# Kernel optimization log

Hardware: AMD Instinct MI355X
Metric: run time of the kernel (lower is better)

Reference implementation:

```python
import jax, jax.numpy as jnp
import numpy as np

IN_CH, OUT_CH, K, DIL = 64, 128, 3, 8

def setup_inputs() -> dict:
    key = jax.random.key(0)
    k1, k2, k3 = jax.random.split(key, 3)
    x = jax.random.normal(k1, (16, IN_CH, 128, 128), dtype=jnp.float32)
    # xavier_normal-like init for W
    fan_in, fan_out = IN_CH * K * K, OUT_CH * K * K
    std = (2.0 / (fan_in + fan_out)) ** 0.5
    W = jax.random.normal(k2, (OUT_CH, IN_CH, K, K), dtype=jnp.float32) * std
    b = jax.random.normal(k3, (OUT_CH,), dtype=jnp.float32)
    return {"x": x, "W": W, "b": b}

def reference(x, W, b):
    pad = DIL * (K // 2)  # circular halo so output spatial size == input
    xp = jnp.pad(x, ((0, 0), (0, 0), (pad, pad), (pad, pad)), mode="wrap")
    y = jax.lax.conv_general_dilated(
        xp, W,
        window_strides=(1, 1),
        padding="VALID",
        rhs_dilation=(DIL, DIL),
        dimension_numbers=("NCHW", "OIHW", "NCHW"),
    )
    return y + b[None, :, None, None]
```

## Files before the change

### kernel.cpp

```cpp
#include <hip/hip_runtime.h>

#define IN_CH 64
#define OUT_CH 128
#define HW 128
#define KTAPS 9
#define ROWB 16384

typedef __bf16 bf16x8 __attribute__((ext_vector_type(8)));
typedef float f32x16 __attribute__((ext_vector_type(16)));
typedef float f32x4 __attribute__((ext_vector_type(4)));

__device__ __forceinline__ unsigned f2bf(float f) {
    unsigned u = __builtin_bit_cast(unsigned, f);
    return (u + 0x7FFFu + ((u >> 16) & 1u)) >> 16;
}

__device__ __forceinline__ unsigned cvt_pk_bf16(float lo, float hi) {
    unsigned r;
    asm("v_cvt_pk_bf16_f32 %0, %1, %2" : "=v"(r) : "v"(lo), "v"(hi));
    return r;
}

__device__ __forceinline__ int swz(int r) { return ((r ^ (r >> 3)) & 7) << 4; }

__global__ void wprep_kernel(const float* __restrict__ W, unsigned short* __restrict__ Wl) {
    int i = blockIdx.x * blockDim.x + threadIdx.x;
    if (i >= OUT_CH * IN_CH * KTAPS) return;
    int p  = i / 36864;
    int r  = i % 36864;
    int t  = r >> 12;
    int r2 = r & 4095;
    int m  = r2 >> 11;
    int ks = (r2 >> 9) & 3;
    int l  = (r2 >> 3) & 63;
    int e  = r2 & 7;
    int oc = p * 64 + m * 32 + (l & 31);
    int ic = ks * 16 + (l >> 5) * 8 + e;
    int kh = t / 3, kw = t % 3;
    Wl[i] = (unsigned short)f2bf(W[((oc * IN_CH + ic) * 3 + kh) * 3 + kw]);
}

#define ISSUE_A(B0, B1, B2, B3, T) do {                                              \
    const char* _pp = (const char*)Ab + (T) * 8192;                                  \
    asm volatile("global_load_dwordx4 %0, %1, off"             : "=v"(B0) : "v"(_pp)); \
    asm volatile("global_load_dwordx4 %0, %1, off offset:1024" : "=v"(B1) : "v"(_pp)); \
    asm volatile("global_load_dwordx4 %0, %1, off offset:2048" : "=v"(B2) : "v"(_pp)); \
    asm volatile("global_load_dwordx4 %0, %1, off offset:3072" : "=v"(B3) : "v"(_pp)); \
} while (0)

#define TAP_BODY(A0_, A1_, A2_, A3_, T, WAITSTR) do {                                \
    constexpr int _kh = (T) / 3, _kw = (T) % 3;                                      \
    int _xc0 = (wc * 64 + l31 + 8 * _kw - 8) & 127;                                  \
    int _xc1 = (_xc0 + 32) & 127;                                                    \
    int _b0 = _kh * ROWB + _xc0 * 128 + lhi * 16, _s0 = swz(_xc0);                   \
    int _b1 = _kh * ROWB + _xc1 * 128 + lhi * 16, _s1 = swz(_xc1);                   \
    asm volatile(WAITSTR);                                                           \
    __builtin_amdgcn_sched_barrier(0);                                               \
    const bf16x8 _A[4] = {A0_, A1_, A2_, A3_};                                       \
    _Pragma("unroll")                                                                \
    for (int ks = 0; ks < 4; ++ks) {                                                 \
        bf16x8 _vb0 = *reinterpret_cast<const bf16x8*>(xsB + ((_b0 + ks * 32) ^ _s0)); \
        bf16x8 _vb1 = *reinterpret_cast<const bf16x8*>(xsB + ((_b1 + ks * 32) ^ _s1)); \
        acc[0] = __builtin_amdgcn_mfma_f32_32x32x16_bf16(_A[ks], _vb0, acc[0], 0, 0, 0); \
        acc[1] = __builtin_amdgcn_mfma_f32_32x32x16_bf16(_A[ks], _vb1, acc[1], 0, 0, 0); \
    }                                                                                \
} while (0)

__global__ __launch_bounds__(512, 5) void conv_kernel_f(
    const float* __restrict__ x, const unsigned short* __restrict__ Wl,
    const float* __restrict__ bias, float* __restrict__ y)
{
    __shared__ __align__(16) unsigned char xsB[3 * ROWB];

    int bid = blockIdx.x;
    int sb  = (bid & 7) * 256 + (bid >> 3);
    int n = sb >> 7, h = sb & 127;
    int tid = threadIdx.x;
    int wid = tid >> 6, lane = tid & 63;

    int wr = wid >> 1, wc = wid & 1;
    int l31 = lane & 31, lhi = lane >> 5;
    int p = wr >> 1, m = wr & 1;

    const bf16x8* Ab = reinterpret_cast<const bf16x8*>(Wl)
                     + p * (9 * 512) + m * 256 + lane;

    bf16x8 aE0, aE1, aE2, aE3, aO0, aO1, aO2, aO3;
    ISSUE_A(aE0, aE1, aE2, aE3, 0);

    #pragma unroll
    for (int g = 0; g < 3; ++g) {
        int q   = g * 512 + tid;
        int w4  = q & 31;
        int ic4 = (q >> 5) & 15;
        int kh  = q >> 9;
        int srow = (h + kh * 8 + 120) & 127;
        const float* xp = x + (((n * IN_CH + ic4 * 4) * HW + srow) * HW + w4 * 4);
        f32x4 v[4];
        #pragma unroll
        for (int j = 0; j < 4; ++j)
            v[j] = *reinterpret_cast<const f32x4*>(xp + j * (HW * HW));
        #pragma unroll
        for (int j2 = 0; j2 < 4; ++j2) {
            int w = w4 * 4 + j2;
            uint2 pk;
            pk.x = cvt_pk_bf16(v[0][j2], v[1][j2]);
            pk.y = cvt_pk_bf16(v[2][j2], v[3][j2]);
            *reinterpret_cast<uint2*>(xsB + kh * ROWB + ((w * 128 + ic4 * 8) ^ swz(w))) = pk;
        }
    }
    __syncthreads();

    f32x16 acc[2];
    #pragma unroll
    for (int bq = 0; bq < 2; ++bq)
        #pragma unroll
        for (int r = 0; r < 16; ++r) acc[bq][r] = 0.0f;

    ISSUE_A(aO0, aO1, aO2, aO3, 1);
    TAP_BODY(aE0, aE1, aE2, aE3, 0, "s_waitcnt vmcnt(4)");
    ISSUE_A(aE0, aE1, aE2, aE3, 2);
    TAP_BODY(aO0, aO1, aO2, aO3, 1, "s_waitcnt vmcnt(4)");
    ISSUE_A(aO0, aO1, aO2, aO3, 3);
    TAP_BODY(aE0, aE1, aE2, aE3, 2, "s_waitcnt vmcnt(4)");
    ISSUE_A(aE0, aE1, aE2, aE3, 4);
    TAP_BODY(aO0, aO1, aO2, aO3, 3, "s_waitcnt vmcnt(4)");
    ISSUE_A(aO0, aO1, aO2, aO3, 5);
    TAP_BODY(aE0, aE1, aE2, aE3, 4, "s_waitcnt vmcnt(4)");
    ISSUE_A(aE0, aE1, aE2, aE3, 6);
    TAP_BODY(aO0, aO1, aO2, aO3, 5, "s_waitcnt vmcnt(4)");
    ISSUE_A(aO0, aO1, aO2, aO3, 7);
    TAP_BODY(aE0, aE1, aE2, aE3, 6, "s_waitcnt vmcnt(4)");
    ISSUE_A(aE0, aE1, aE2, aE3, 8);
    TAP_BODY(aO0, aO1, aO2, aO3, 7, "s_waitcnt vmcnt(4)");
    TAP_BODY(aE0, aE1, aE2, aE3, 8, "s_waitcnt vmcnt(0)");

    int outbase = (n * OUT_CH) * HW * HW + h * HW;
    #pragma unroll
    for (int bq = 0; bq < 2; ++bq) {
        int wcol = wc * 64 + bq * 32 + l31;
        #pragma unroll
        for (int reg = 0; reg < 16; ++reg) {
            int oc = wr * 32 + (reg & 3) + 8 * (reg >> 2) + 4 * lhi;
            y[outbase + oc * HW * HW + wcol] = acc[bq][reg] + bias[oc];
        }
    }
}

extern "C" void kernel_launch(void* const* d_in, const int* in_sizes, int n_in,
                              void* d_out, int out_size, void* d_ws, size_t ws_size,
                              hipStream_t stream) {
    const float* x = (const float*)d_in[0];
    const float* W = (const float*)d_in[1];
    const float* b = (const float*)d_in[2];
    float* y = (float*)d_out;

    unsigned short* Wl = (unsigned short*)d_ws;

    hipLaunchKernelGGL(wprep_kernel, dim3((OUT_CH * IN_CH * KTAPS + 255) / 256), dim3(256), 0, stream, W, Wl);
    hipLaunchKernelGGL(conv_kernel_f, dim3(16 * HW), dim3(512), 0, stream, x, Wl, b, y);
}
```

Measured before the change: 61.22 us.

## Split each output row into two half-row blocks with an 80-column halo tile

```diff
diff --git a/kernel.cpp b/kernel.cpp
--- a/kernel.cpp
+++ b/kernel.cpp
@@ -4,7 +4,8 @@
 #define OUT_CH 128
 #define HW 128
 #define KTAPS 9
-#define ROWB 16384
+#define LCOLS 80
+#define LROWB (LCOLS * 128)
 
 typedef __bf16 bf16x8 __attribute__((ext_vector_type(8)));
 typedef float f32x16 __attribute__((ext_vector_type(16)));
@@ -50,10 +51,10 @@
 
 #define TAP_BODY(A0_, A1_, A2_, A3_, T, WAITSTR) do {                                \
     constexpr int _kh = (T) / 3, _kw = (T) % 3;                                      \
-    int _xc0 = (wc * 64 + l31 + 8 * _kw - 8) & 127;                                  \
-    int _xc1 = (_xc0 + 32) & 127;                                                    \
-    int _b0 = _kh * ROWB + _xc0 * 128 + lhi * 16, _s0 = swz(_xc0);                   \
-    int _b1 = _kh * ROWB + _xc1 * 128 + lhi * 16, _s1 = swz(_xc1);                   \
+    int _xc0 = l31 + 8 * _kw;                                                        \
+    int _xc1 = _xc0 + 32;                                                            \
+    int _b0 = _kh * LROWB + _xc0 * 128 + lhi * 16, _s0 = swz(_xc0);                  \
+    int _b1 = _kh * LROWB + _xc1 * 128 + lhi * 16, _s1 = swz(_xc1);                  \
     asm volatile(WAITSTR);                                                           \
     __builtin_amdgcn_sched_barrier(0);                                               \
     const bf16x8 _A[4] = {A0_, A1_, A2_, A3_};                                       \
@@ -66,47 +67,47 @@
     }                                                                                \
 } while (0)
 
-__global__ __launch_bounds__(512, 5) void conv_kernel_f(
+__global__ __launch_bounds__(256, 4) void conv_kernel_f(
     const float* __restrict__ x, const unsigned short* __restrict__ Wl,
     const float* __restrict__ bias, float* __restrict__ y)
 {
-    __shared__ __align__(16) unsigned char xsB[3 * ROWB];
+    __shared__ __align__(16) unsigned char xsB[40960];
 
     int bid = blockIdx.x;
-    int sb  = (bid & 7) * 256 + (bid >> 3);
-    int n = sb >> 7, h = sb & 127;
-    int tid = threadIdx.x;
-    int wid = tid >> 6, lane = tid & 63;
-
-    int wr = wid >> 1, wc = wid & 1;
+    int sb  = (bid & 7) * 512 + (bid >> 3);
+    int half = sb & 1;
+    int h    = (sb >> 1) & 127;
+    int n    = sb >> 8;
+    int w0   = half * 64;
+    int tid  = threadIdx.x;
+    int wid  = tid >> 6, lane = tid & 63;
     int l31 = lane & 31, lhi = lane >> 5;
-    int p = wr >> 1, m = wr & 1;
 
     const bf16x8* Ab = reinterpret_cast<const bf16x8*>(Wl)
-                     + p * (9 * 512) + m * 256 + lane;
+                     + (wid >> 1) * (9 * 512) + (wid & 1) * 256 + lane;
 
     bf16x8 aE0, aE1, aE2, aE3, aO0, aO1, aO2, aO3;
     ISSUE_A(aE0, aE1, aE2, aE3, 0);
 
-    #pragma unroll
-    for (int g = 0; g < 3; ++g) {
-        int q   = g * 512 + tid;
-        int w4  = q & 31;
-        int ic4 = (q >> 5) & 15;
-        int kh  = q >> 9;
-        int srow = (h + kh * 8 + 120) & 127;
-        const float* xp = x + (((n * IN_CH + ic4 * 4) * HW + srow) * HW + w4 * 4);
+    for (int q = tid; q < 960; q += 256) {
+        int ic4 = q & 15;
+        int c5  = q >> 4;
+        int c4  = c5 % 20;
+        int row = c5 / 20;
+        int srow = (h + row * 8 + 120) & 127;
+        int g4   = (w0 - 8 + c4 * 4) & 127;
+        const float* xp = x + (((n * IN_CH + ic4 * 4) * HW + srow) * HW + g4);
         f32x4 v[4];
         #pragma unroll
         for (int j = 0; j < 4; ++j)
             v[j] = *reinterpret_cast<const f32x4*>(xp + j * (HW * HW));
         #pragma unroll
         for (int j2 = 0; j2 < 4; ++j2) {
-            int w = w4 * 4 + j2;
+            int lc = c4 * 4 + j2;
             uint2 pk;
             pk.x = cvt_pk_bf16(v[0][j2], v[1][j2]);
             pk.y = cvt_pk_bf16(v[2][j2], v[3][j2]);
-            *reinterpret_cast<uint2*>(xsB + kh * ROWB + ((w * 128 + ic4 * 8) ^ swz(w))) = pk;
+            *reinterpret_cast<uint2*>(xsB + row * LROWB + ((lc * 128 + ic4 * 8) ^ swz(lc))) = pk;
         }
     }
     __syncthreads();
@@ -138,10 +139,10 @@
     int outbase = (n * OUT_CH) * HW * HW + h * HW;
     #pragma unroll
     for (int bq = 0; bq < 2; ++bq) {
-        int wcol = wc * 64 + bq * 32 + l31;
+        int wcol = w0 + bq * 32 + l31;
         #pragma unroll
         for (int reg = 0; reg < 16; ++reg) {
-            int oc = wr * 32 + (reg & 3) + 8 * (reg >> 2) + 4 * lhi;
+            int oc = wid * 32 + (reg & 3) + 8 * (reg >> 2) + 4 * lhi;
             y[outbase + oc * HW * HW + wcol] = acc[bq][reg] + bias[oc];
         }
     }
@@ -158,5 +159,5 @@
     unsigned short* Wl = (unsigned short*)d_ws;
 
     hipLaunchKernelGGL(wprep_kernel, dim3((OUT_CH * IN_CH * KTAPS + 255) / 256), dim3(256), 0, stream, W, Wl);
-    hipLaunchKernelGGL(conv_kernel_f, dim3(16 * HW), dim3(512), 0, stream, x, Wl, b, y);
+    hipLaunchKernelGGL(conv_kernel_f, dim3(4096), dim3(256), 0, stream, x, Wl, b, y);
 }
```

Measured after the change: 77.54 us. +26.7%, slower.
